# Performance work log

Hardware: AMD Instinct MI355X
Metric: run time of the kernel (lower is better)

## Reference

```python
import jax, jax.numpy as jnp
import numpy as np

C = 1024
RANK = 8


def _layernorm(x, g, b, eps=1e-5):
    mu = jnp.mean(x, axis=-1, keepdims=True)
    var = jnp.var(x, axis=-1, keepdims=True)
    return (x - mu) * jax.lax.rsqrt(var + eps) * g + b


def setup_inputs() -> dict:
    key = jax.random.key(0)
    ks = jax.random.split(key, 10)
    B, T = 4, 4096
    x = jax.random.normal(ks[0], (B, T, C), dtype=jnp.float32)
    # parameters (match torch inits)
    W0 = jnp.eye(C, dtype=jnp.float32) * 0.1
    A_init = jax.random.normal(ks[1], (C, RANK), dtype=jnp.float32) * 0.01
    B_init = jnp.zeros((RANK, C), dtype=jnp.float32)
    log_lr = jnp.full((C,), float(np.log(0.1)), dtype=jnp.float32)
    s = 1.0 / np.sqrt(C)
    Wq = jax.random.uniform(ks[2], (C, C), minval=-s, maxval=s, dtype=jnp.float32)
    Wk = jax.random.uniform(ks[3], (C, C), minval=-s, maxval=s, dtype=jnp.float32)
    Wv = jax.random.uniform(ks[4], (C, C), minval=-s, maxval=s, dtype=jnp.float32)
    Wo = jax.random.uniform(ks[5], (C, C), minval=-s, maxval=s, dtype=jnp.float32)
    Wg = jax.random.uniform(ks[6], (C, C), minval=-s, maxval=s, dtype=jnp.float32)
    ln_g = jnp.ones((C,), dtype=jnp.float32)
    ln_b = jnp.zeros((C,), dtype=jnp.float32)
    ls_g = jnp.full((C,), 1e-4, dtype=jnp.float32)  # LayerScale gamma
    return {"x": x, "W0": W0, "A_init": A_init, "B_init": B_init,
            "log_lr": log_lr, "Wq": Wq, "Wk": Wk, "Wv": Wv, "Wo": Wo,
            "Wg": Wg, "ln_g": ln_g, "ln_b": ln_b, "ls_g": ls_g}


def reference(x, W0, A_init, B_init, log_lr, Wq, Wk, Wv, Wo, Wg, ln_g, ln_b, ls_g):
    B, T, _ = x.shape
    h = _layernorm(x, ln_g, ln_b)
    # dual-form TTT (training path: q/k/v projections, full K @ W0)
    Q = jnp.einsum('btc,dc->btd', h, Wq)
    K = jnp.einsum('btc,dc->btd', h, Wk)
    V = jnp.einsum('btc,dc->btd', h, Wv)
    lr = jnp.minimum(jnp.exp(log_lr), 1.0)  # clamp(max=1.0)
    y0 = jnp.einsum('btc,cd->btd', K, W0) + jnp.einsum('btr,rd->btd', jnp.einsum('btc,cr->btr', K, A_init), B_init)
    error = y0 - V
    loss = jnp.mean(error ** 2)
    gradient = K * error                     # [B,T,C]
    grad_cumsum = jnp.cumsum(gradient, axis=1)
    grad_shift = jnp.concatenate([jnp.zeros((B, 1, gradient.shape[-1]), gradient.dtype), grad_cumsum[:, :-1, :]], axis=1)
    correction = Q * lr[None, None, :] * grad_shift
    pos = jnp.arange(1, T + 1, dtype=correction.dtype)
    pos_scale = (1.0 / (1.0 + 0.1 * jnp.log(pos)))[None, :, None]
    out = y0 - correction * pos_scale
    # gate, out projection, layer scale, residual
    gate = jax.nn.sigmoid(jnp.einsum('btc,dc->btd', x, Wg))
    out = out * gate
    out = jnp.einsum('btc,dc->btd', out, Wo) * ls_g
    return (x + out, loss)
```

## Files before the change

kernel.cpp:

```cpp
#include <hip/hip_runtime.h>
#include <stdint.h>
#include <math.h>

typedef unsigned short u16;
typedef __attribute__((ext_vector_type(8))) short short8;
typedef __attribute__((ext_vector_type(4))) float f32x4;

__device__ __forceinline__ float bf2f(u16 u){
  union { unsigned int i; float f; } v; v.i = ((unsigned int)u) << 16; return v.f;
}
__device__ __forceinline__ u16 f2bf(float f){
  union { float f; unsigned int i; } v; v.f = f;
  return (u16)((v.i + 0x7FFFu + ((v.i >> 16) & 1u)) >> 16);
}

__global__ void ln_prep(const float* __restrict__ x, const float* __restrict__ g,
                        const float* __restrict__ bta, u16* __restrict__ h,
                        u16* __restrict__ xb, float* __restrict__ loss){
  if (blockIdx.x == 0 && threadIdx.x == 0) loss[0] = 0.f;
  int row = blockIdx.x, tid = threadIdx.x;
  const float4* xr = (const float4*)(x + (size_t)row * 1024);
  float4 v = xr[tid];
  float s  = v.x + v.y + v.z + v.w;
  float s2 = v.x*v.x + v.y*v.y + v.z*v.z + v.w*v.w;
  #pragma unroll
  for (int o = 32; o > 0; o >>= 1){ s += __shfl_down(s, o); s2 += __shfl_down(s2, o); }
  __shared__ float red[8];
  if ((tid & 63) == 0){ red[tid >> 6] = s; red[4 + (tid >> 6)] = s2; }
  __syncthreads();
  float ts = red[0]+red[1]+red[2]+red[3];
  float t2 = red[4]+red[5]+red[6]+red[7];
  float mu   = ts * (1.0f/1024.0f);
  float var  = t2 * (1.0f/1024.0f) - mu*mu;
  float rstd = rsqrtf(var + 1e-5f);
  float4 gg = ((const float4*)g)[tid];
  float4 bb = ((const float4*)bta)[tid];
  ushort4 hv, xv;
  hv.x = f2bf((v.x-mu)*rstd*gg.x + bb.x);
  hv.y = f2bf((v.y-mu)*rstd*gg.y + bb.y);
  hv.z = f2bf((v.z-mu)*rstd*gg.z + bb.z);
  hv.w = f2bf((v.w-mu)*rstd*gg.w + bb.w);
  xv.x = f2bf(v.x); xv.y = f2bf(v.y); xv.z = f2bf(v.z); xv.w = f2bf(v.w);
  ((ushort4*)h )[(size_t)row*256 + tid] = hv;
  ((ushort4*)xb)[(size_t)row*256 + tid] = xv;
}

__global__ void conv5(const float* __restrict__ a, const float* __restrict__ b,
                      const float* __restrict__ c, const float* __restrict__ d,
                      const float* __restrict__ e,
                      u16* oa, u16* ob, u16* oc, u16* od, u16* oe){
  int sel = blockIdx.y;
  const float* s = sel==0?a : sel==1?b : sel==2?c : sel==3?d : e;
  u16* o = sel==0?oa : sel==1?ob : sel==2?oc : sel==3?od : oe;
  int i = blockIdx.x*256 + threadIdx.x;
  float4 v = ((const float4*)s)[i];
  ushort4 r; r.x=f2bf(v.x); r.y=f2bf(v.y); r.z=f2bf(v.z); r.w=f2bf(v.w);
  ((ushort4*)o)[i] = r;
}

__global__ void weff_k(const float* __restrict__ W0, const float* __restrict__ Ai,
                       const float* __restrict__ Bi, u16* __restrict__ Wet){
  __shared__ float tile[32][33];
  int d0 = blockIdx.x*32, e0 = blockIdx.y*32;
  int tid = threadIdx.x;
  int lr = tid >> 5, lc = tid & 31;
  #pragma unroll
  for (int s = 0; s < 4; ++s){
    int e = e0 + s*8 + lr, d = d0 + lc;
    float v = W0[(size_t)e*1024 + d];
    #pragma unroll
    for (int r = 0; r < 8; ++r) v += Ai[e*8 + r] * Bi[(size_t)r*1024 + d];
    tile[s*8 + lr][lc] = v;
  }
  __syncthreads();
  #pragma unroll
  for (int s = 0; s < 4; ++s){
    int d = d0 + s*8 + lr, e = e0 + lc;
    Wet[(size_t)d*1024 + e] = f2bf(tile[lc][s*8 + lr]);
  }
}

__global__ void psk(float* __restrict__ psg){
  int t = blockIdx.x*256 + threadIdx.x;
  psg[t] = 1.0f/(1.0f + 0.1f*logf((float)(t+1)));
}

template<int EPI>
__device__ __forceinline__ void gemm_body(const u16* __restrict__ A, const u16* __restrict__ Bm,
    u16* __restrict__ Cb, float* __restrict__ Cf, const float* __restrict__ lsg,
    const float* __restrict__ xres,
    const u16* __restrict__ Kb2, const u16* __restrict__ Vb2,
    u16* __restrict__ Gr, float* __restrict__ part, float* __restrict__ loss,
    int mblk, int nblk){
  __shared__ u16 As[128*64];
  __shared__ u16 Bs[128*64];
  const int tid  = threadIdx.x;
  const int lane = tid & 63;
  const int w    = tid >> 6;
  const int m0 = mblk * 128, n0 = nblk * 128;
  const int lrow = lane >> 3;
  const int gcol8 = (((lane & 7) ^ (lrow & 7)) * 8);
  const int wm = w & 1, wn = w >> 1;
  const int l15 = lane & 15, quad = lane >> 4;
  const int sw  = (l15 & 7);

  f32x4 acc[4][4] = {};

  #pragma unroll 1
  for (int kk = 0; kk < 1024; kk += 64){
    #pragma unroll
    for (int it = 0; it < 4; ++it){
      int r0 = w*8 + it*32;
      const u16* ga = A  + (size_t)(m0 + r0 + lrow)*1024 + kk + gcol8;
      __builtin_amdgcn_global_load_lds((const __attribute__((address_space(1))) unsigned int*)ga,
          (__attribute__((address_space(3))) unsigned int*)(As + r0*64), 16, 0, 0);
      const u16* gb = Bm + (size_t)(n0 + r0 + lrow)*1024 + kk + gcol8;
      __builtin_amdgcn_global_load_lds((const __attribute__((address_space(1))) unsigned int*)gb,
          (__attribute__((address_space(3))) unsigned int*)(Bs + r0*64), 16, 0, 0);
    }
    __syncthreads();
    #pragma unroll
    for (int kh = 0; kh < 2; ++kh){
      int kbi = kh*4 + quad;
      int koff = ((kbi ^ sw) * 8);
      short8 af[4], bfv[4];
      #pragma unroll
      for (int i = 0; i < 4; ++i) af[i]  = *(const short8*)(As + (wm*64 + i*16 + l15)*64 + koff);
      #pragma unroll
      for (int j = 0; j < 4; ++j) bfv[j] = *(const short8*)(Bs + (wn*64 + j*16 + l15)*64 + koff);
      #pragma unroll
      for (int i = 0; i < 4; ++i)
        #pragma unroll
        for (int j = 0; j < 4; ++j)
          acc[i][j] = __builtin_amdgcn_mfma_f32_16x16x32_bf16(af[i], bfv[j], acc[i][j], 0, 0, 0);
    }
    __syncthreads();
  }

  const int rbase = quad * 4;
  if (EPI == 0){
    #pragma unroll
    for (int i = 0; i < 4; ++i){
      int row = m0 + wm*64 + i*16 + rbase;
      #pragma unroll
      for (int j = 0; j < 4; ++j){
        int col = n0 + wn*64 + j*16 + l15;
        #pragma unroll
        for (int r = 0; r < 4; ++r)
          Cb[(size_t)(row + r)*1024 + col] = f2bf(acc[i][j][r]);
      }
    }
  } else if (EPI == 1){
    float lsv[4];
    #pragma unroll
    for (int j = 0; j < 4; ++j) lsv[j] = lsg[n0 + wn*64 + j*16 + l15];
    #pragma unroll
    for (int i = 0; i < 4; ++i){
      int row = m0 + wm*64 + i*16 + rbase;
      #pragma unroll
      for (int j = 0; j < 4; ++j){
        int col = n0 + wn*64 + j*16 + l15;
        #pragma unroll
        for (int r = 0; r < 4; ++r){
          size_t idx = (size_t)(row + r)*1024 + col;
          Cf[idx] = acc[i][j][r] * lsv[j] + xres[idx];
        }
      }
    }
  } else {
    float csum[4] = {0.f, 0.f, 0.f, 0.f};
    float ls = 0.f;
    #pragma unroll
    for (int i = 0; i < 4; ++i){
      int row = m0 + wm*64 + i*16 + rbase;
      #pragma unroll
      for (int j = 0; j < 4; ++j){
        int col = n0 + wn*64 + j*16 + l15;
        #pragma unroll
        for (int r = 0; r < 4; ++r){
          size_t idx = (size_t)(row + r)*1024 + col;
          float y  = acc[i][j][r];
          float kv = bf2f(Kb2[idx]);
          float vv = bf2f(Vb2[idx]);
          float e  = y - vv;
          float gv = kv * e;
          Cb[idx] = f2bf(y);
          Gr[idx] = f2bf(gv);
          csum[j] += gv;
          ls += e * e;
        }
      }
    }
    #pragma unroll
    for (int j = 0; j < 4; ++j){
      csum[j] += __shfl_xor(csum[j], 16);
      csum[j] += __shfl_xor(csum[j], 32);
    }
    float* cr = (float*)As;
    if (quad == 0){
      #pragma unroll
      for (int j = 0; j < 4; ++j) cr[wm*128 + wn*64 + j*16 + l15] = csum[j];
    }
    #pragma unroll
    for (int o = 32; o > 0; o >>= 1) ls += __shfl_down(ls, o);
    if (lane == 0) cr[256 + w] = ls;
    __syncthreads();
    if (tid < 128) part[(size_t)mblk * 1024 + n0 + tid] = cr[tid] + cr[128 + tid];
    if (tid == 0) atomicAdd(loss, cr[256]+cr[257]+cr[258]+cr[259]);
  }
}

__global__ void gemm_qkvg(const u16* __restrict__ h, const u16* __restrict__ xb,
                          const u16* __restrict__ Wqb, const u16* __restrict__ Wkb,
                          const u16* __restrict__ Wvb, const u16* __restrict__ Wgb,
                          u16* __restrict__ Qb, u16* __restrict__ Kb,
                          u16* __restrict__ Vb, u16* __restrict__ Gb){
  int sel = blockIdx.y >> 3;
  const u16* A  = (sel == 3) ? xb : h;
  const u16* Bm = sel==0?Wqb : sel==1?Wkb : sel==2?Wvb : Wgb;
  u16* Out      = sel==0?Qb  : sel==1?Kb  : sel==2?Vb  : Gb;
  gemm_body<0>(A, Bm, Out, nullptr, nullptr, nullptr,
               nullptr, nullptr, nullptr, nullptr, nullptr, blockIdx.x, blockIdx.y & 7);
}

__global__ void gemm_y0(const u16* __restrict__ Kb, const u16* __restrict__ Wet,
                        u16* __restrict__ Yb, const u16* __restrict__ Vb,
                        u16* __restrict__ Gr, float* __restrict__ part,
                        float* __restrict__ loss){
  gemm_body<2>(Kb, Wet, Yb, nullptr, nullptr, nullptr,
               Kb, Vb, Gr, part, loss, blockIdx.x, blockIdx.y);
}

__global__ void gemm_final(const u16* __restrict__ A, const u16* __restrict__ Bm,
                           float* __restrict__ C, const float* __restrict__ lsg,
                           const float* __restrict__ xres){
  gemm_body<1>(A, Bm, nullptr, C, lsg, xres,
               nullptr, nullptr, nullptr, nullptr, nullptr, blockIdx.x, blockIdx.y);
}

__global__ void scan2(const u16* __restrict__ Gr, const u16* __restrict__ Yb,
                      const u16* __restrict__ Qb, const u16* __restrict__ Gb,
                      const float* __restrict__ part, const float* __restrict__ llr,
                      const float* __restrict__ psg, u16* __restrict__ OutPre){
  int tid = threadIdx.x;
  int c2  = blockIdx.x*128 + tid;
  int ch = blockIdx.y, b = blockIdx.z;
  __shared__ float ps_s[128];
  ps_s[tid] = psg[ch*128 + tid];
  int c = c2*2;
  float run0 = 0.f, run1 = 0.f;
  for (int j = 0; j < ch; ++j){
    float2 pp = *(const float2*)(part + ((size_t)(b*32 + j))*1024 + c);
    run0 += pp.x; run1 += pp.y;
  }
  float2 lr2 = *(const float2*)(llr + c);
  float lrc0 = fminf(expf(lr2.x), 1.0f);
  float lrc1 = fminf(expf(lr2.y), 1.0f);
  __syncthreads();
  size_t base = ((size_t)b*4096 + (size_t)ch*128)*512 + c2;
  const ushort2* Gr2 = (const ushort2*)Gr;
  const ushort2* Yb2 = (const ushort2*)Yb;
  const ushort2* Qb2 = (const ushort2*)Qb;
  const ushort2* Gb2 = (const ushort2*)Gb;
  ushort2* Ot2 = (ushort2*)OutPre;
  #pragma unroll 8
  for (int t = 0; t < 128; ++t){
    size_t idx = base + (size_t)t*512;
    ushort2 gr = Gr2[idx], yv = Yb2[idx], qv = Qb2[idx], gl = Gb2[idx];
    float ps = ps_s[t];
    float g0 = 1.0f/(1.0f + expf(-bf2f(gl.x)));
    float g1 = 1.0f/(1.0f + expf(-bf2f(gl.y)));
    float o0 = (bf2f(yv.x) - bf2f(qv.x)*lrc0*run0*ps) * g0;
    float o1 = (bf2f(yv.y) - bf2f(qv.y)*lrc1*run1*ps) * g1;
    ushort2 ov; ov.x = f2bf(o0); ov.y = f2bf(o1);
    Ot2[idx] = ov;
    run0 += bf2f(gr.x); run1 += bf2f(gr.y);
  }
}

__global__ void finloss(const float* __restrict__ loss, float* __restrict__ o){
  o[0] = loss[0] * (1.0f/16777216.0f);
}

extern "C" void kernel_launch(void* const* d_in, const int* in_sizes, int n_in,
                              void* d_out, int out_size, void* d_ws, size_t ws_size,
                              hipStream_t stream){
  const float* x   = (const float*)d_in[0];
  const float* W0  = (const float*)d_in[1];
  const float* Ai  = (const float*)d_in[2];
  const float* Bi  = (const float*)d_in[3];
  const float* llr = (const float*)d_in[4];
  const float* Wq  = (const float*)d_in[5];
  const float* Wk  = (const float*)d_in[6];
  const float* Wv  = (const float*)d_in[7];
  const float* Wo  = (const float*)d_in[8];
  const float* Wg  = (const float*)d_in[9];
  const float* lng = (const float*)d_in[10];
  const float* lnb = (const float*)d_in[11];
  const float* lsg = (const float*)d_in[12];
  float* out = (float*)d_out;

  const size_t TOK = 16384, CC = 1024;
  char* p = (char*)d_ws;
  float* loss = (float*)p; p += 256;
  u16* h   = (u16*)p; p += TOK*CC*2;
  u16* xb  = (u16*)p; p += TOK*CC*2;
  u16* Qb  = (u16*)p; p += TOK*CC*2;
  u16* Kb  = (u16*)p; p += TOK*CC*2;
  u16* Vb  = (u16*)p; p += TOK*CC*2;
  u16* Gb  = (u16*)p; p += TOK*CC*2;
  u16* Wqb = (u16*)p; p += CC*CC*2;
  u16* Wkb = (u16*)p; p += CC*CC*2;
  u16* Wvb = (u16*)p; p += CC*CC*2;
  u16* Wgb = (u16*)p; p += CC*CC*2;
  u16* Wob = (u16*)p; p += CC*CC*2;
  u16* Wet = (u16*)p; p += CC*CC*2;
  float* part = (float*)p; p += (size_t)128*1024*4;
  float* psg  = (float*)p; p += 4096*4;

  ln_prep<<<16384, 256, 0, stream>>>(x, lng, lnb, h, xb, loss);
  conv5<<<dim3(1024, 5), 256, 0, stream>>>(Wq, Wk, Wv, Wg, Wo, Wqb, Wkb, Wvb, Wgb, Wob);
  weff_k<<<dim3(32, 32), 256, 0, stream>>>(W0, Ai, Bi, Wet);
  psk<<<16, 256, 0, stream>>>(psg);
  gemm_qkvg<<<dim3(128, 32), 256, 0, stream>>>(h, xb, Wqb, Wkb, Wvb, Wgb, Qb, Kb, Vb, Gb);
  gemm_y0<<<dim3(128, 8), 256, 0, stream>>>(Kb, Wet, h, Vb, xb, part, loss);
  scan2<<<dim3(4, 32, 4), 128, 0, stream>>>(xb, h, Qb, Gb, part, llr, psg, Qb);
  gemm_final<<<dim3(128, 8), 256, 0, stream>>>(Qb, Wob, out, lsg, x);
  finloss<<<1, 1, 0, stream>>>(loss, out + 16777216);
}
```

Before: 523.1 us.

## Split y0 epilogue into scan kernel, merge prep kernels, stage final epilogue via LDS

Merges the weight conversion, effective-weight and position-scale kernels into one prep launch, and also precomputes the clamped learning rate there. The gradient and loss epilogue is moved out of the y0 GEMM into a separate scan1 kernel, so the GEMM writes plain bf16 output. The final GEMM epilogue now stages the accumulators through shared memory so residual reads and output writes use coalesced float4 accesses. The trade-off is an extra kernel that rereads K, V and Y0 from memory, in exchange for a lighter GEMM epilogue and fewer uncoalesced stores.

```diff
diff --git a/kernel.cpp b/kernel.cpp
--- a/kernel.cpp
+++ b/kernel.cpp
@@ -45,55 +45,57 @@
   ((ushort4*)xb)[(size_t)row*256 + tid] = xv;
 }
 
-__global__ void conv5(const float* __restrict__ a, const float* __restrict__ b,
-                      const float* __restrict__ c, const float* __restrict__ d,
-                      const float* __restrict__ e,
-                      u16* oa, u16* ob, u16* oc, u16* od, u16* oe){
-  int sel = blockIdx.y;
-  const float* s = sel==0?a : sel==1?b : sel==2?c : sel==3?d : e;
-  u16* o = sel==0?oa : sel==1?ob : sel==2?oc : sel==3?od : oe;
-  int i = blockIdx.x*256 + threadIdx.x;
-  float4 v = ((const float4*)s)[i];
-  ushort4 r; r.x=f2bf(v.x); r.y=f2bf(v.y); r.z=f2bf(v.z); r.w=f2bf(v.w);
-  ((ushort4*)o)[i] = r;
-}
-
-__global__ void weff_k(const float* __restrict__ W0, const float* __restrict__ Ai,
-                       const float* __restrict__ Bi, u16* __restrict__ Wet){
-  __shared__ float tile[32][33];
-  int d0 = blockIdx.x*32, e0 = blockIdx.y*32;
-  int tid = threadIdx.x;
-  int lr = tid >> 5, lc = tid & 31;
-  #pragma unroll
-  for (int s = 0; s < 4; ++s){
-    int e = e0 + s*8 + lr, d = d0 + lc;
-    float v = W0[(size_t)e*1024 + d];
-    #pragma unroll
-    for (int r = 0; r < 8; ++r) v += Ai[e*8 + r] * Bi[(size_t)r*1024 + d];
-    tile[s*8 + lr][lc] = v;
-  }
-  __syncthreads();
-  #pragma unroll
-  for (int s = 0; s < 4; ++s){
-    int d = d0 + s*8 + lr, e = e0 + lc;
-    Wet[(size_t)d*1024 + e] = f2bf(tile[lc][s*8 + lr]);
-  }
-}
-
-__global__ void psk(float* __restrict__ psg){
-  int t = blockIdx.x*256 + threadIdx.x;
-  psg[t] = 1.0f/(1.0f + 0.1f*logf((float)(t+1)));
+__global__ void prep_misc(const float* __restrict__ Wq, const float* __restrict__ Wk,
+                          const float* __restrict__ Wv, const float* __restrict__ Wg,
+                          const float* __restrict__ Wo, const float* __restrict__ W0,
+                          const float* __restrict__ Ai, const float* __restrict__ Bi,
+                          const float* __restrict__ llr,
+                          u16* __restrict__ Wqb, u16* __restrict__ Wkb,
+                          u16* __restrict__ Wvb, u16* __restrict__ Wgb,
+                          u16* __restrict__ Wob, u16* __restrict__ Wet,
+                          float* __restrict__ psg, float* __restrict__ lrc){
+  int bx = blockIdx.x, tid = threadIdx.x;
+  if (bx < 5120){
+    int sel = bx >> 10;
+    const float* s = sel==0?Wq : sel==1?Wk : sel==2?Wv : sel==3?Wg : Wo;
+    u16* o = sel==0?Wqb : sel==1?Wkb : sel==2?Wvb : sel==3?Wgb : Wob;
+    int i = (bx & 1023)*256 + tid;
+    float4 v = ((const float4*)s)[i];
+    ushort4 r; r.x=f2bf(v.x); r.y=f2bf(v.y); r.z=f2bf(v.z); r.w=f2bf(v.w);
+    ((ushort4*)o)[i] = r;
+  } else if (bx < 6144){
+    __shared__ float tile[32][33];
+    int wb = bx - 5120;
+    int d0 = (wb & 31)*32, e0 = (wb >> 5)*32;
+    int lr = tid >> 5, lc = tid & 31;
+    #pragma unroll
+    for (int s = 0; s < 4; ++s){
+      int e = e0 + s*8 + lr, d = d0 + lc;
+      float v = W0[(size_t)e*1024 + d];
+      #pragma unroll
+      for (int r = 0; r < 8; ++r) v += Ai[e*8 + r] * Bi[(size_t)r*1024 + d];
+      tile[s*8 + lr][lc] = v;
+    }
+    __syncthreads();
+    #pragma unroll
+    for (int s = 0; s < 4; ++s){
+      int d = d0 + s*8 + lr, e = e0 + lc;
+      Wet[(size_t)d*1024 + e] = f2bf(tile[lc][s*8 + lr]);
+    }
+  } else {
+    int t = (bx - 6144)*256 + tid;
+    psg[t] = 1.0f/(1.0f + 0.1f*logf((float)(t+1)));
+    if (t < 1024) lrc[t] = fminf(expf(llr[t]), 1.0f);
+  }
 }
 
 template<int EPI>
 __device__ __forceinline__ void gemm_body(const u16* __restrict__ A, const u16* __restrict__ Bm,
     u16* __restrict__ Cb, float* __restrict__ Cf, const float* __restrict__ lsg,
-    const float* __restrict__ xres,
-    const u16* __restrict__ Kb2, const u16* __restrict__ Vb2,
-    u16* __restrict__ Gr, float* __restrict__ part, float* __restrict__ loss,
-    int mblk, int nblk){
-  __shared__ u16 As[128*64];
-  __shared__ u16 Bs[128*64];
+    const float* __restrict__ xres, int mblk, int nblk){
+  __shared__ u16 smem[16384];
+  u16* As = smem;
+  u16* Bs = smem + 8192;
   const int tid  = threadIdx.x;
   const int lane = tid & 63;
   const int w    = tid >> 6;
@@ -150,63 +152,33 @@
           Cb[(size_t)(row + r)*1024 + col] = f2bf(acc[i][j][r]);
       }
     }
-  } else if (EPI == 1){
-    float lsv[4];
-    #pragma unroll
-    for (int j = 0; j < 4; ++j) lsv[j] = lsg[n0 + wn*64 + j*16 + l15];
+  } else {
+    float* cf = (float*)smem;
+    const int lr = tid >> 3, seg = tid & 7;
+    float4 lsv[4];
+    #pragma unroll
+    for (int k = 0; k < 4; ++k) lsv[k] = *(const float4*)(lsg + n0 + seg*16 + k*4);
     #pragma unroll
     for (int i = 0; i < 4; ++i){
-      int row = m0 + wm*64 + i*16 + rbase;
-      #pragma unroll
-      for (int j = 0; j < 4; ++j){
-        int col = n0 + wn*64 + j*16 + l15;
+      __syncthreads();
+      #pragma unroll
+      for (int j = 0; j < 4; ++j)
         #pragma unroll
-        for (int r = 0; r < 4; ++r){
-          size_t idx = (size_t)(row + r)*1024 + col;
-          Cf[idx] = acc[i][j][r] * lsv[j] + xres[idx];
-        }
+        for (int r = 0; r < 4; ++r)
+          cf[(wm*16 + rbase + r)*132 + wn*64 + j*16 + l15] = acc[i][j][r];
+      __syncthreads();
+      int grow = m0 + i*16 + (lr & 15) + (lr >> 4)*64;
+      size_t gbase = (size_t)grow*1024 + n0 + seg*16;
+      #pragma unroll
+      for (int k = 0; k < 4; ++k){
+        float4 o = *(const float4*)(cf + lr*132 + seg*16 + k*4);
+        float4 xr = *(const float4*)(xres + gbase + k*4);
+        float4 res;
+        res.x = o.x*lsv[k].x + xr.x; res.y = o.y*lsv[k].y + xr.y;
+        res.z = o.z*lsv[k].z + xr.z; res.w = o.w*lsv[k].w + xr.w;
+        *(float4*)(Cf + gbase + k*4) = res;
       }
     }
-  } else {
-    float csum[4] = {0.f, 0.f, 0.f, 0.f};
-    float ls = 0.f;
-    #pragma unroll
-    for (int i = 0; i < 4; ++i){
-      int row = m0 + wm*64 + i*16 + rbase;
-      #pragma unroll
-      for (int j = 0; j < 4; ++j){
-        int col = n0 + wn*64 + j*16 + l15;
-        #pragma unroll
-        for (int r = 0; r < 4; ++r){
-          size_t idx = (size_t)(row + r)*1024 + col;
-          float y  = acc[i][j][r];
-          float kv = bf2f(Kb2[idx]);
-          float vv = bf2f(Vb2[idx]);
-          float e  = y - vv;
-          float gv = kv * e;
-          Cb[idx] = f2bf(y);
-          Gr[idx] = f2bf(gv);
-          csum[j] += gv;
-          ls += e * e;
-        }
-      }
-    }
-    #pragma unroll
-    for (int j = 0; j < 4; ++j){
-      csum[j] += __shfl_xor(csum[j], 16);
-      csum[j] += __shfl_xor(csum[j], 32);
-    }
-    float* cr = (float*)As;
-    if (quad == 0){
-      #pragma unroll
-      for (int j = 0; j < 4; ++j) cr[wm*128 + wn*64 + j*16 + l15] = csum[j];
-    }
-    #pragma unroll
-    for (int o = 32; o > 0; o >>= 1) ls += __shfl_down(ls, o);
-    if (lane == 0) cr[256 + w] = ls;
-    __syncthreads();
-    if (tid < 128) part[(size_t)mblk * 1024 + n0 + tid] = cr[tid] + cr[128 + tid];
-    if (tid == 0) atomicAdd(loss, cr[256]+cr[257]+cr[258]+cr[259]);
   }
 }
 
@@ -219,28 +191,56 @@
   const u16* A  = (sel == 3) ? xb : h;
   const u16* Bm = sel==0?Wqb : sel==1?Wkb : sel==2?Wvb : Wgb;
   u16* Out      = sel==0?Qb  : sel==1?Kb  : sel==2?Vb  : Gb;
-  gemm_body<0>(A, Bm, Out, nullptr, nullptr, nullptr,
-               nullptr, nullptr, nullptr, nullptr, nullptr, blockIdx.x, blockIdx.y & 7);
+  gemm_body<0>(A, Bm, Out, nullptr, nullptr, nullptr, blockIdx.x, blockIdx.y & 7);
 }
 
 __global__ void gemm_y0(const u16* __restrict__ Kb, const u16* __restrict__ Wet,
-                        u16* __restrict__ Yb, const u16* __restrict__ Vb,
-                        u16* __restrict__ Gr, float* __restrict__ part,
-                        float* __restrict__ loss){
-  gemm_body<2>(Kb, Wet, Yb, nullptr, nullptr, nullptr,
-               Kb, Vb, Gr, part, loss, blockIdx.x, blockIdx.y);
+                        u16* __restrict__ Yb){
+  gemm_body<0>(Kb, Wet, Yb, nullptr, nullptr, nullptr, blockIdx.x, blockIdx.y);
 }
 
 __global__ void gemm_final(const u16* __restrict__ A, const u16* __restrict__ Bm,
                            float* __restrict__ C, const float* __restrict__ lsg,
                            const float* __restrict__ xres){
-  gemm_body<1>(A, Bm, nullptr, C, lsg, xres,
-               nullptr, nullptr, nullptr, nullptr, nullptr, blockIdx.x, blockIdx.y);
+  gemm_body<1>(A, Bm, nullptr, C, lsg, xres, blockIdx.x, blockIdx.y);
+}
+
+__global__ void scan1(const u16* __restrict__ Kb, const u16* __restrict__ Vb,
+                      const u16* __restrict__ Yb, u16* __restrict__ Gr,
+                      float* __restrict__ part, float* __restrict__ loss){
+  int tid = threadIdx.x;
+  int c2  = blockIdx.x*128 + tid;
+  int ch = blockIdx.y, b = blockIdx.z;
+  size_t base = ((size_t)b*4096 + (size_t)ch*128)*512 + c2;
+  const ushort2* K2 = (const ushort2*)Kb;
+  const ushort2* V2 = (const ushort2*)Vb;
+  const ushort2* Y2 = (const ushort2*)Yb;
+  ushort2* G2 = (ushort2*)Gr;
+  float g0 = 0.f, g1 = 0.f, ls = 0.f;
+  #pragma unroll 8
+  for (int t = 0; t < 128; ++t){
+    size_t idx = base + (size_t)t*512;
+    ushort2 kv = K2[idx], vv = V2[idx], yv = Y2[idx];
+    float e0 = bf2f(yv.x) - bf2f(vv.x);
+    float e1 = bf2f(yv.y) - bf2f(vv.y);
+    float gv0 = bf2f(kv.x)*e0, gv1 = bf2f(kv.y)*e1;
+    ushort2 gw; gw.x = f2bf(gv0); gw.y = f2bf(gv1);
+    G2[idx] = gw;
+    g0 += gv0; g1 += gv1; ls += e0*e0 + e1*e1;
+  }
+  float2 pw; pw.x = g0; pw.y = g1;
+  *(float2*)(part + ((size_t)(b*32 + ch))*1024 + c2*2) = pw;
+  #pragma unroll
+  for (int o = 32; o > 0; o >>= 1) ls += __shfl_down(ls, o);
+  __shared__ float red[2];
+  if ((tid & 63) == 0) red[tid >> 6] = ls;
+  __syncthreads();
+  if (tid == 0) atomicAdd(loss, red[0] + red[1]);
 }
 
 __global__ void scan2(const u16* __restrict__ Gr, const u16* __restrict__ Yb,
                       const u16* __restrict__ Qb, const u16* __restrict__ Gb,
-                      const float* __restrict__ part, const float* __restrict__ llr,
+                      const float* __restrict__ part, const float* __restrict__ lrc,
                       const float* __restrict__ psg, u16* __restrict__ OutPre){
   int tid = threadIdx.x;
   int c2  = blockIdx.x*128 + tid;
@@ -253,9 +253,7 @@
     float2 pp = *(const float2*)(part + ((size_t)(b*32 + j))*1024 + c);
     run0 += pp.x; run1 += pp.y;
   }
-  float2 lr2 = *(const float2*)(llr + c);
-  float lrc0 = fminf(expf(lr2.x), 1.0f);
-  float lrc1 = fminf(expf(lr2.y), 1.0f);
+  float2 lr2 = *(const float2*)(lrc + c);
   __syncthreads();
   size_t base = ((size_t)b*4096 + (size_t)ch*128)*512 + c2;
   const ushort2* Gr2 = (const ushort2*)Gr;
@@ -270,8 +268,8 @@
     float ps = ps_s[t];
     float g0 = 1.0f/(1.0f + expf(-bf2f(gl.x)));
     float g1 = 1.0f/(1.0f + expf(-bf2f(gl.y)));
-    float o0 = (bf2f(yv.x) - bf2f(qv.x)*lrc0*run0*ps) * g0;
-    float o1 = (bf2f(yv.y) - bf2f(qv.y)*lrc1*run1*ps) * g1;
+    float o0 = (bf2f(yv.x) - bf2f(qv.x)*lr2.x*run0*ps) * g0;
+    float o1 = (bf2f(yv.y) - bf2f(qv.y)*lr2.y*run1*ps) * g1;
     ushort2 ov; ov.x = f2bf(o0); ov.y = f2bf(o1);
     Ot2[idx] = ov;
     run0 += bf2f(gr.x); run1 += bf2f(gr.y);
@@ -315,16 +313,17 @@
   u16* Wgb = (u16*)p; p += CC*CC*2;
   u16* Wob = (u16*)p; p += CC*CC*2;
   u16* Wet = (u16*)p; p += CC*CC*2;
+  float* psg  = (float*)p; p += 4096*4;
+  float* lrc  = (float*)p; p += 1024*4;
   float* part = (float*)p; p += (size_t)128*1024*4;
-  float* psg  = (float*)p; p += 4096*4;
 
   ln_prep<<<16384, 256, 0, stream>>>(x, lng, lnb, h, xb, loss);
-  conv5<<<dim3(1024, 5), 256, 0, stream>>>(Wq, Wk, Wv, Wg, Wo, Wqb, Wkb, Wvb, Wgb, Wob);
-  weff_k<<<dim3(32, 32), 256, 0, stream>>>(W0, Ai, Bi, Wet);
-  psk<<<16, 256, 0, stream>>>(psg);
+  prep_misc<<<6160, 256, 0, stream>>>(Wq, Wk, Wv, Wg, Wo, W0, Ai, Bi, llr,
+                                      Wqb, Wkb, Wvb, Wgb, Wob, Wet, psg, lrc);
   gemm_qkvg<<<dim3(128, 32), 256, 0, stream>>>(h, xb, Wqb, Wkb, Wvb, Wgb, Qb, Kb, Vb, Gb);
-  gemm_y0<<<dim3(128, 8), 256, 0, stream>>>(Kb, Wet, h, Vb, xb, part, loss);
-  scan2<<<dim3(4, 32, 4), 128, 0, stream>>>(xb, h, Qb, Gb, part, llr, psg, Qb);
+  gemm_y0<<<dim3(128, 8), 256, 0, stream>>>(Kb, Wet, h);
+  scan1<<<dim3(4, 32, 4), 128, 0, stream>>>(Kb, Vb, h, xb, part, loss);
+  scan2<<<dim3(4, 32, 4), 128, 0, stream>>>(xb, h, Qb, Gb, part, lrc, psg, Qb);
   gemm_final<<<dim3(128, 8), 256, 0, stream>>>(Qb, Wob, out, lsg, x);
   finloss<<<1, 1, 0, stream>>>(loss, out + 16777216);
 }
```

Result: no change. 517.9 us (-1.0%).
